# Kernel optimization log

Measured on AMD Instinct MI355X. Metric: run time of the kernel, lower is better.

## Reference

```python
import jax, jax.numpy as jnp
import numpy as np
from jax import lax

B, S, T = 256, 128, 64
IN, MID, HID = 4, 128, 512
NH = 4  # attention heads


def setup_inputs() -> dict:
    key = jax.random.key(0)
    ks = iter(jax.random.split(key, 64))
    def p(*shape):
        return jax.random.normal(next(ks), shape, jnp.float32) * 0.05
    d = {}
    d["src"] = jax.random.normal(next(ks), (B, S, IN), jnp.float32)
    d["trg"] = jax.random.normal(next(ks), (B, T, IN), jnp.float32)
    # fc_in: IN -> MID//4 -> MID//2 -> MID
    d["fi_w1"] = p(MID // 4, IN); d["fi_b1"] = p(MID // 4)
    d["fi_w2"] = p(MID // 2, MID // 4); d["fi_b2"] = p(MID // 2)
    d["fi_w3"] = p(MID, MID // 2); d["fi_b3"] = p(MID)
    # encoder: 2-layer bidirectional LSTM (layer0 in=MID, layer1 in=2*HID)
    for name, ind in [("e0", MID), ("e1", 2 * HID)]:
        for sfx in ["f", "b"]:
            d[name + sfx + "_wih"] = p(4 * HID, ind)
            d[name + sfx + "_whh"] = p(4 * HID, HID)
            d[name + sfx + "_bih"] = p(4 * HID)
            d[name + sfx + "_bhh"] = p(4 * HID)
    d["attnfc_w"] = p(MID, 2 * HID); d["attnfc_b"] = p(MID)
    d["inproj_w"] = p(3 * MID, MID); d["inproj_b"] = p(3 * MID)
    d["outproj_w"] = p(MID, MID); d["outproj_b"] = p(MID)
    # decoder: 2-layer unidirectional LSTM (layer0 in=MID, layer1 in=HID)
    for name, ind in [("d0", MID), ("d1", HID)]:
        d[name + "_wih"] = p(4 * HID, ind)
        d[name + "_whh"] = p(4 * HID, HID)
        d[name + "_bih"] = p(4 * HID)
        d[name + "_bhh"] = p(4 * HID)
    # fc_out: HID -> MID//2 -> MID//4 -> IN
    d["fo_w1"] = p(MID // 2, HID); d["fo_b1"] = p(MID // 2)
    d["fo_w2"] = p(MID // 4, MID // 2); d["fo_b2"] = p(MID // 4)
    d["fo_w3"] = p(IN, MID // 4); d["fo_b3"] = p(IN)
    return d


def _gelu(x):
    return jax.nn.gelu(x, approximate=False)  # torch default GELU is exact


def _mlp3(x, w1, b1, w2, b2, w3, b3):
    h = _gelu(x @ w1.T + b1)
    h = _gelu(h @ w2.T + b2)
    return h @ w3.T + b3


def _lstm(x, h0, c0, wih, whh, bih, bhh, reverse=False):
    """PyTorch-semantics LSTM layer. x: (B,T,in) -> (hs (B,T,H), h_T, c_T)."""
    xg = jnp.einsum('bti,gi->btg', x, wih) + (bih + bhh)  # fold input GEMM over time
    def step(carry, xt):
        h, c = carry
        g = xt + h @ whh.T
        i, f, gg, o = jnp.split(g, 4, axis=-1)  # torch gate order: i,f,g,o
        c = jax.nn.sigmoid(f) * c + jax.nn.sigmoid(i) * jnp.tanh(gg)
        h = jax.nn.sigmoid(o) * jnp.tanh(c)
        return (h, c), h
    (h, c), hs = lax.scan(step, (h0, c0), jnp.swapaxes(xg, 0, 1), reverse=reverse)
    return jnp.swapaxes(hs, 0, 1), h, c


def _mha(q_in, kv, inproj_w, inproj_b, outproj_w, outproj_b):
    E = q_in.shape[-1]
    dh = E // NH
    wq, wk, wv = jnp.split(inproj_w, 3, axis=0)
    bq, bk, bv = jnp.split(inproj_b, 3)
    q = q_in @ wq.T + bq
    k = kv @ wk.T + bk
    v = kv @ wv.T + bv
    hd = lambda x: x.reshape(x.shape[0], x.shape[1], NH, dh)
    scores = jnp.einsum('bqhd,bkhd->bhqk', hd(q), hd(k)) * (1.0 / float(np.sqrt(dh)))
    a = jax.nn.softmax(scores, axis=-1)
    o = jnp.einsum('bhqk,bkhd->bqhd', a, hd(v)).reshape(q.shape)
    return o @ outproj_w.T + outproj_b


def reference(src, trg,
              fi_w1, fi_b1, fi_w2, fi_b2, fi_w3, fi_b3,
              e0f_wih, e0f_whh, e0f_bih, e0f_bhh, e0b_wih, e0b_whh, e0b_bih, e0b_bhh,
              e1f_wih, e1f_whh, e1f_bih, e1f_bhh, e1b_wih, e1b_whh, e1b_bih, e1b_bhh,
              attnfc_w, attnfc_b, inproj_w, inproj_b, outproj_w, outproj_b,
              d0_wih, d0_whh, d0_bih, d0_bhh, d1_wih, d1_whh, d1_bih, d1_bhh,
              fo_w1, fo_b1, fo_w2, fo_b2, fo_w3, fo_b3):
    bsz = src.shape[0]
    z = jnp.zeros((bsz, HID), src.dtype)
    enc_embed = _mlp3(src, fi_w1, fi_b1, fi_w2, fi_b2, fi_w3, fi_b3)
    # encoder layer 0 (bidirectional)
    l0f, hf0, cf0 = _lstm(enc_embed, z, z, e0f_wih, e0f_whh, e0f_bih, e0f_bhh)
    l0b, hb0, cb0 = _lstm(enc_embed, z, z, e0b_wih, e0b_whh, e0b_bih, e0b_bhh, reverse=True)
    x1 = jnp.concatenate([l0f, l0b], axis=-1)
    # encoder layer 1 (bidirectional)
    l1f, hf1, cf1 = _lstm(x1, z, z, e1f_wih, e1f_whh, e1f_bih, e1f_bhh)
    l1b, hb1, cb1 = _lstm(x1, z, z, e1b_wih, e1b_whh, e1b_bih, e1b_bhh, reverse=True)
    enc_out = jnp.concatenate([l1f, l1b], axis=-1)  # (B,S,2H)
    # h.view(L,2,B,H).sum(dim=1): sum forward+backward final states per layer
    h_l0, c_l0 = hf0 + hb0, cf0 + cb0
    h_l1, c_l1 = hf1 + hb1, cf1 + cb1
    proj_enc = jnp.tanh(enc_out @ attnfc_w.T + attnfc_b)  # (B,S,MID)
    # teacher_forcing_ratio = 1.0 -> decoder inputs are exactly trg[:, 0:T]
    inp = _mlp3(trg, fi_w1, fi_b1, fi_w2, fi_b2, fi_w3, fi_b3)  # (B,T,MID)
    attn_out = _mha(inp, proj_enc, inproj_w, inproj_b, outproj_w, outproj_b)
    dec_input = inp + attn_out
    d0, _, _ = _lstm(dec_input, h_l0, c_l0, d0_wih, d0_whh, d0_bih, d0_bhh)
    d1, _, _ = _lstm(d0, h_l1, c_l1, d1_wih, d1_whh, d1_bih, d1_bhh)
    delta = _mlp3(d1, fo_w1, fo_b1, fo_w2, fo_b2, fo_w3, fo_b3)
    return trg + delta  # pred_t = trg[:, t-1] + delta_t
```

## Files before the change

### kernel.cpp

```cpp
#include <hip/hip_runtime.h>
#include <cstdint>
#include <cstddef>
#include <cstdio>

typedef __bf16 bf16;
typedef __bf16 bf16x8 __attribute__((ext_vector_type(8)));
typedef __bf16 bf16x4 __attribute__((ext_vector_type(4)));
typedef float f32x4 __attribute__((ext_vector_type(4)));

#define DEVFN __device__ __forceinline__

DEVFN float geluf(float x) { return 0.5f * x * (1.0f + erff(x * 0.70710678118654752f)); }
DEVFN float sigmoidf(float x) { return 1.0f / (1.0f + expf(-x)); }

template <int WGM, int WGN, int ACT, bool RES>
__launch_bounds__(WGM * WGN * 64)
__global__ void gemm_bt(const bf16* __restrict__ A, const bf16* __restrict__ W,
                        const float* __restrict__ bias, const bf16* __restrict__ Rsd,
                        bf16* __restrict__ C, int M, int N, int K) {
  constexpr int BM = WGM * 64, BN = WGN * 64, T = WGM * WGN * 64;
  constexpr int NA = BM * 4 / T, NB = BN * 4 / T;
  __shared__ __align__(16) char ldsA[BM * 64];
  __shared__ __align__(16) char ldsB[BN * 64];
  const int tid = threadIdx.x;
  const int lane = tid & 63, wave = tid >> 6;
  const int wm = wave % WGM, wn = wave / WGM;
  const int l16 = lane & 15, quad = lane >> 4;
  const int bm0 = blockIdx.x * BM, bn0 = blockIdx.y * BN;

  f32x4 acc[4][4] = {};
  for (int k0 = 0; k0 < K; k0 += 32) {
    bf16x8 ta[NA], tb[NB];
#pragma unroll
    for (int i = 0; i < NA; ++i) {
      int lin = i * T + tid;
      int row = lin >> 2, seg = lin & 3;
      ta[i] = *(const bf16x8*)(A + (size_t)(bm0 + row) * K + k0 + seg * 8);
    }
#pragma unroll
    for (int i = 0; i < NB; ++i) {
      int lin = i * T + tid;
      int row = lin >> 2, seg = lin & 3;
      tb[i] = *(const bf16x8*)(W + (size_t)(bn0 + row) * K + k0 + seg * 8);
    }
#pragma unroll
    for (int i = 0; i < NA; ++i) *(bf16x8*)(ldsA + (i * T + tid) * 16) = ta[i];
#pragma unroll
    for (int i = 0; i < NB; ++i) *(bf16x8*)(ldsB + (i * T + tid) * 16) = tb[i];
    __syncthreads();
    bf16x8 af[4], bfrag[4];
#pragma unroll
    for (int mi = 0; mi < 4; ++mi)
      af[mi] = *(const bf16x8*)(ldsA + (wm * 64 + mi * 16 + l16) * 64 + quad * 16);
#pragma unroll
    for (int ni = 0; ni < 4; ++ni)
      bfrag[ni] = *(const bf16x8*)(ldsB + (wn * 64 + ni * 16 + l16) * 64 + quad * 16);
#pragma unroll
    for (int mi = 0; mi < 4; ++mi)
#pragma unroll
      for (int ni = 0; ni < 4; ++ni)
        acc[mi][ni] = __builtin_amdgcn_mfma_f32_16x16x32_bf16(af[mi], bfrag[ni], acc[mi][ni], 0, 0, 0);
    __syncthreads();
  }
#pragma unroll
  for (int mi = 0; mi < 4; ++mi) {
#pragma unroll
    for (int ni = 0; ni < 4; ++ni) {
      int col = bn0 + wn * 64 + ni * 16 + l16;
      float bv = bias[col];
#pragma unroll
      for (int r = 0; r < 4; ++r) {
        int row = bm0 + wm * 64 + mi * 16 + quad * 4 + r;
        float x = acc[mi][ni][r] + bv;
        if (ACT == 1) x = tanhf(x);
        if (ACT == 2) x = geluf(x);
        size_t idx = (size_t)row * N + col;
        if (RES) x += (float)Rsd[idx];
        C[idx] = (bf16)x;
      }
    }
  }
}

template <int WGM, int WGN, int ACT>
__launch_bounds__(WGM * WGN * 64)
__global__ void gemm_hcA(const bf16* __restrict__ HC, int tbase, const bf16* __restrict__ W,
                         const float* __restrict__ bias, bf16* __restrict__ C,
                         int M, int N, int K) {
  constexpr int BM = WGM * 64, BN = WGN * 64, T = WGM * WGN * 64;
  constexpr int NA = BM * 4 / T, NB = BN * 4 / T;
  __shared__ __align__(16) char ldsA[BM * 64];
  __shared__ __align__(16) char ldsB[BN * 64];
  const int tid = threadIdx.x;
  const int lane = tid & 63, wave = tid >> 6;
  const int wm = wave % WGM, wn = wave / WGM;
  const int l16 = lane & 15, quad = lane >> 4;
  const int bm0 = blockIdx.x * BM, bn0 = blockIdx.y * BN;

  f32x4 acc[4][4] = {};
  for (int k0 = 0; k0 < K; k0 += 32) {
    bf16x8 ta[NA], tb[NB];
#pragma unroll
    for (int i = 0; i < NA; ++i) {
      int lin = i * T + tid;
      int row = bm0 + (lin >> 2), seg = lin & 3;
      int t = tbase + (row >> 8), b = row & 255;
      ta[i] = *(const bf16x8*)(HC + (size_t)t * 262144 + (size_t)((k0 >> 3) + seg) * 2048 + b * 8);
    }
#pragma unroll
    for (int i = 0; i < NB; ++i) {
      int lin = i * T + tid;
      int row = lin >> 2, seg = lin & 3;
      tb[i] = *(const bf16x8*)(W + (size_t)(bn0 + row) * K + k0 + seg * 8);
    }
#pragma unroll
    for (int i = 0; i < NA; ++i) *(bf16x8*)(ldsA + (i * T + tid) * 16) = ta[i];
#pragma unroll
    for (int i = 0; i < NB; ++i) *(bf16x8*)(ldsB + (i * T + tid) * 16) = tb[i];
    __syncthreads();
    bf16x8 af[4], bfrag[4];
#pragma unroll
    for (int mi = 0; mi < 4; ++mi)
      af[mi] = *(const bf16x8*)(ldsA + (wm * 64 + mi * 16 + l16) * 64 + quad * 16);
#pragma unroll
    for (int ni = 0; ni < 4; ++ni)
      bfrag[ni] = *(const bf16x8*)(ldsB + (wn * 64 + ni * 16 + l16) * 64 + quad * 16);
#pragma unroll
    for (int mi = 0; mi < 4; ++mi)
#pragma unroll
      for (int ni = 0; ni < 4; ++ni)
        acc[mi][ni] = __builtin_amdgcn_mfma_f32_16x16x32_bf16(af[mi], bfrag[ni], acc[mi][ni], 0, 0, 0);
    __syncthreads();
  }
#pragma unroll
  for (int mi = 0; mi < 4; ++mi) {
#pragma unroll
    for (int ni = 0; ni < 4; ++ni) {
      int col = bn0 + wn * 64 + ni * 16 + l16;
      float bv = bias[col];
#pragma unroll
      for (int r = 0; r < 4; ++r) {
        int row = bm0 + wm * 64 + mi * 16 + quad * 4 + r;
        float x = acc[mi][ni][r] + bv;
        if (ACT == 1) x = tanhf(x);
        if (ACT == 2) x = geluf(x);
        C[(size_t)row * N + col] = (bf16)x;
      }
    }
  }
}

__launch_bounds__(128)
__global__ void gemm_hc_fcout(const bf16* __restrict__ HC, const bf16* __restrict__ W,
                              const float* __restrict__ bias, bf16* __restrict__ C,
                              int M, int N, int K) {
  constexpr int WGM = 2, WGN = 1;
  constexpr int BM = WGM * 64, BN = WGN * 64, T = WGM * WGN * 64;
  constexpr int NA = BM * 4 / T, NB = BN * 4 / T;
  __shared__ __align__(16) char ldsA[BM * 64];
  __shared__ __align__(16) char ldsB[BN * 64];
  const int tid = threadIdx.x;
  const int lane = tid & 63, wave = tid >> 6;
  const int wm = wave % WGM, wn = wave / WGM;
  const int l16 = lane & 15, quad = lane >> 4;
  const int bm0 = blockIdx.x * BM, bn0 = blockIdx.y * BN;

  f32x4 acc[4][4] = {};
  for (int k0 = 0; k0 < K; k0 += 32) {
    bf16x8 ta[NA], tb[NB];
#pragma unroll
    for (int i = 0; i < NA; ++i) {
      int lin = i * T + tid;
      int row = bm0 + (lin >> 2), seg = lin & 3;
      int t = row >> 8, b = row & 255;
      ta[i] = *(const bf16x8*)(HC + (size_t)t * 131072 + (size_t)((k0 >> 3) + seg) * 2048 + b * 8);
    }
#pragma unroll
    for (int i = 0; i < NB; ++i) {
      int lin = i * T + tid;
      int row = lin >> 2, seg = lin & 3;
      tb[i] = *(const bf16x8*)(W + (size_t)(bn0 + row) * K + k0 + seg * 8);
    }
#pragma unroll
    for (int i = 0; i < NA; ++i) *(bf16x8*)(ldsA + (i * T + tid) * 16) = ta[i];
#pragma unroll
    for (int i = 0; i < NB; ++i) *(bf16x8*)(ldsB + (i * T + tid) * 16) = tb[i];
    __syncthreads();
    bf16x8 af[4], bfrag[4];
#pragma unroll
    for (int mi = 0; mi < 4; ++mi)
      af[mi] = *(const bf16x8*)(ldsA + (wm * 64 + mi * 16 + l16) * 64 + quad * 16);
#pragma unroll
    for (int ni = 0; ni < 4; ++ni)
      bfrag[ni] = *(const bf16x8*)(ldsB + (wn * 64 + ni * 16 + l16) * 64 + quad * 16);
#pragma unroll
    for (int mi = 0; mi < 4; ++mi)
#pragma unroll
      for (int ni = 0; ni < 4; ++ni)
        acc[mi][ni] = __builtin_amdgcn_mfma_f32_16x16x32_bf16(af[mi], bfrag[ni], acc[mi][ni], 0, 0, 0);
    __syncthreads();
  }
#pragma unroll
  for (int mi = 0; mi < 4; ++mi) {
#pragma unroll
    for (int ni = 0; ni < 4; ++ni) {
      int col = bn0 + wn * 64 + ni * 16 + l16;
      float bv = bias[col];
#pragma unroll
      for (int r = 0; r < 4; ++r) {
        int row = bm0 + wm * 64 + mi * 16 + quad * 4 + r;
        float x = geluf(acc[mi][ni][r] + bv);
        C[(size_t)row * N + col] = (bf16)x;
      }
    }
  }
}

template <int HCMODE>
DEVFN void xg_tile(const bf16* __restrict__ A, int tbase, const bf16* __restrict__ W,
                   const float* __restrict__ bias, bf16* __restrict__ C,
                   int K, int bm0, int bn0, int tid, bf16* ldsA, bf16* ldsB) {
  const int lane = tid & 63, wave = tid >> 6;
  const int wm = wave & 1, wn = wave >> 1;
  const int l16 = lane & 15, quad = lane >> 4;
  f32x4 acc[4][4] = {};
  for (int k0 = 0; k0 < K; k0 += 32) {
    bf16x8 ta, tb0, tb1;
    {
      int row = bm0 + (tid >> 2), seg = tid & 3;
      if (HCMODE) {
        int t = tbase + (row >> 8), b = row & 255;
        ta = *(const bf16x8*)(A + (size_t)t * 262144 + (size_t)((k0 >> 3) + seg) * 2048 + b * 8);
      } else {
        ta = *(const bf16x8*)(A + (size_t)row * K + k0 + seg * 8);
      }
    }
    { int row = tid >> 2, seg = tid & 3;
      tb0 = *(const bf16x8*)(W + (size_t)(bn0 + row) * K + k0 + seg * 8); }
    { int lin = 512 + tid; int row = lin >> 2, seg = lin & 3;
      tb1 = *(const bf16x8*)(W + (size_t)(bn0 + row) * K + k0 + seg * 8); }
    *(bf16x8*)(ldsA + tid * 8) = ta;
    *(bf16x8*)(ldsB + tid * 8) = tb0;
    *(bf16x8*)(ldsB + (512 + tid) * 8) = tb1;
    __syncthreads();
    bf16x8 af[4], bfr[4];
#pragma unroll
    for (int mi = 0; mi < 4; ++mi)
      af[mi] = *(const bf16x8*)(ldsA + (wm * 64 + mi * 16 + l16) * 32 + quad * 8);
#pragma unroll
    for (int ni = 0; ni < 4; ++ni)
      bfr[ni] = *(const bf16x8*)(ldsB + (wn * 64 + ni * 16 + l16) * 32 + quad * 8);
#pragma unroll
    for (int mi = 0; mi < 4; ++mi)
#pragma unroll
      for (int ni = 0; ni < 4; ++ni)
        acc[mi][ni] = __builtin_amdgcn_mfma_f32_16x16x32_bf16(af[mi], bfr[ni], acc[mi][ni], 0, 0, 0);
    __syncthreads();
  }
#pragma unroll
  for (int mi = 0; mi < 4; ++mi) {
#pragma unroll
    for (int ni = 0; ni < 4; ++ni) {
      int col = bn0 + wn * 64 + ni * 16 + l16;
      float bv = bias[col];
#pragma unroll
      for (int r = 0; r < 4; ++r) {
        int row = bm0 + wm * 64 + mi * 16 + quad * 4 + r;
        C[(size_t)row * 2048 + col] = (bf16)(acc[mi][ni][r] + bv);
      }
    }
  }
}

struct RDir {
  const bf16* whh_r;
  const bf16* xg;
  bf16* hc;
  int slcOff, rev;
  const bf16* h0;
  float* cbuf;
  bf16* hfin;
};

struct GJob {
  int mode;
  const bf16* Af; const bf16* Ab;
  int tbF, tbB;
  const bf16* Wf; const bf16* Wb;
  const float* bsF; const float* bsB;
  bf16* outF; bf16* outB;
};

__launch_bounds__(512, 1)
__global__ void lstm_rec_g(RDir da, RDir db, int t0, int tc, int Tfull,
                           int* __restrict__ cnts, GJob job) {
  __shared__ __align__(16) char smem[36864];
  const int blk = blockIdx.x;
  const int tid = threadIdx.x;

  if (blk >= 128) {
    if (job.mode == 0) return;
    bf16* ldsA = (bf16*)smem;
    bf16* ldsB = (bf16*)(smem + 8192);
    const int gb = blk - 128;
    const int K = (job.mode == 2) ? 1024 : 128;
    for (int tile = gb; tile < 512; tile += 128) {
      int dir = tile >> 8;
      int rem = tile & 255;
      int mi = rem >> 3, ni = rem & 7;
      const bf16* A = dir ? job.Ab : job.Af;
      int tb = dir ? job.tbB : job.tbF;
      const bf16* W = dir ? job.Wb : job.Wf;
      const float* bs = dir ? job.bsB : job.bsF;
      bf16* C = dir ? job.outB : job.outF;
      if (job.mode == 2)
        xg_tile<1>(A, tb, W, bs, C, K, mi * 128, ni * 256, tid, ldsA, ldsB);
      else
        xg_tile<0>(A, tb, W, bs, C, K, mi * 128, ni * 256, tid, ldsA, ldsB);
    }
    return;
  }

  bf16* whh_lds = (bf16*)smem;
  bf16* hstg = (bf16*)(smem + 32768);
  const RDir d = (blk >= 64) ? db : da;
  const int slice = blk & 63;
  const int colBase = slice * 32, unitBase = slice * 8;
  const int w = tid >> 6, lane = tid & 63;
  const int l16 = lane & 15, quad = lane >> 4;

  for (int e = tid * 8; e < 32 * 512; e += 512 * 8) {
    int c = e >> 9, k0 = e & 511;
    bf16x8 v = *(const bf16x8*)(d.whh_r + (size_t)(colBase + c) * 512 + k0);
    *(bf16x8*)(whh_lds + ((k0 >> 3) << 8) + (c << 3)) = v;
  }
  float cst[2][2];
#pragma unroll
  for (int m = 0; m < 2; ++m)
#pragma unroll
    for (int i = 0; i < 2; ++i) {
      int b = (w * 2 + i) * 16 + l16;
      cst[m][i] = d.cbuf[(size_t)b * 512 + unitBase + m * 4 + quad];
    }
  __syncthreads();

  int* cnt = cnts + (blk & 64);
  const int b0 = (w * 2) * 16 + l16;
  const int b1 = b0 + 16;

  for (int s = 0; s < tc; ++s) {
    const int sg = t0 + s;
    const int t = d.rev ? (Tfull - 1 - sg) : sg;
    const int lt = d.rev ? (tc - 1 - s) : s;

    bf16x4 gxr[2][2];
#pragma unroll
    for (int m = 0; m < 2; ++m)
#pragma unroll
      for (int i = 0; i < 2; ++i) {
        int b = b0 + i * 16;
        gxr[m][i] = *(const bf16x4*)(d.xg + ((size_t)lt * 256 + b) * 2048 + colBase + m * 16 + quad * 4);
      }
    bf16x8 hr[16][2];
    if (sg == 0) {
      const bf16* hp0 = d.h0 + (size_t)b0 * 512 + quad * 8;
      const bf16* hp1 = d.h0 + (size_t)b1 * 512 + quad * 8;
#pragma unroll
      for (int kk = 0; kk < 16; ++kk) {
        hr[kk][0] = *(const bf16x8*)(hp0 + kk * 32);
        hr[kk][1] = *(const bf16x8*)(hp1 + kk * 32);
      }
    } else {
      const int tp = d.rev ? (t + 1) : (t - 1);
      const bf16* hc = d.hc + (size_t)tp * 262144 + (size_t)d.slcOff * 2048;
#pragma unroll
      for (int kk = 0; kk < 16; ++kk) {
        int u8 = kk * 4 + quad;
        hr[kk][0] = *(const bf16x8*)(hc + u8 * 2048 + (size_t)b0 * 8);
        hr[kk][1] = *(const bf16x8*)(hc + u8 * 2048 + (size_t)b1 * 8);
      }
    }
    __builtin_amdgcn_sched_barrier(0);

    f32x4 acc[2][2] = {};
#pragma unroll
    for (int kk = 0; kk < 16; ++kk) {
      bf16x8 a0 = *(const bf16x8*)(whh_lds + kk * 1024 + quad * 256 + l16 * 8);
      bf16x8 a1 = *(const bf16x8*)(whh_lds + kk * 1024 + quad * 256 + 128 + l16 * 8);
      acc[0][0] = __builtin_amdgcn_mfma_f32_16x16x32_bf16(a0, hr[kk][0], acc[0][0], 0, 0, 0);
      acc[1][0] = __builtin_amdgcn_mfma_f32_16x16x32_bf16(a1, hr[kk][0], acc[1][0], 0, 0, 0);
      acc[0][1] = __builtin_amdgcn_mfma_f32_16x16x32_bf16(a0, hr[kk][1], acc[0][1], 0, 0, 0);
      acc[1][1] = __builtin_amdgcn_mfma_f32_16x16x32_bf16(a1, hr[kk][1], acc[1][1], 0, 0, 0);
    }
#pragma unroll
    for (int m = 0; m < 2; ++m)
#pragma unroll
      for (int i = 0; i < 2; ++i) {
        float gi = acc[m][i][0] + (float)gxr[m][i][0];
        float gf = acc[m][i][1] + (float)gxr[m][i][1];
        float gg = acc[m][i][2] + (float)gxr[m][i][2];
        float go = acc[m][i][3] + (float)gxr[m][i][3];
        float cn = sigmoidf(gf) * cst[m][i] + sigmoidf(gi) * tanhf(gg);
        float hv = sigmoidf(go) * tanhf(cn);
        cst[m][i] = cn;
        int b = (w * 2 + i) * 16 + l16;
        hstg[b * 8 + m * 4 + quad] = (bf16)hv;
      }
    __syncthreads();
    {
      unsigned long long v = *(const unsigned long long*)(hstg + tid * 4);
      __hip_atomic_store((unsigned long long*)(d.hc + (size_t)t * 262144 +
                                               (size_t)(d.slcOff + slice) * 2048 + tid * 4),
                         v, __ATOMIC_RELAXED, __HIP_MEMORY_SCOPE_AGENT);
    }
    __syncthreads();
    if (s < tc - 1 && tid == 0)
      __hip_atomic_fetch_add(cnt, 1, __ATOMIC_RELAXED, __HIP_MEMORY_SCOPE_AGENT);
    if (sg == Tfull - 1 && d.hfin && tid < 256) {
      const unsigned long long* p = (const unsigned long long*)(hstg + tid * 8);
      unsigned long long* r2 = (unsigned long long*)(d.hfin + (size_t)tid * 512 + unitBase);
      r2[0] = p[0]; r2[1] = p[1];
    }
    if (s < tc - 1) {
      if (w == 0) {
        int target = 64 * (s + 1), guard = 0;
        while (__hip_atomic_load(cnt, __ATOMIC_RELAXED, __HIP_MEMORY_SCOPE_AGENT) < target) {
          __builtin_amdgcn_s_sleep(2);
          if (++guard > (1 << 22)) break;
        }
      }
      __syncthreads();
    }
  }
#pragma unroll
  for (int m = 0; m < 2; ++m)
#pragma unroll
    for (int i = 0; i < 2; ++i) {
      int b = (w * 2 + i) * 16 + l16;
      d.cbuf[(size_t)b * 512 + unitBase + m * 4 + quad] = cst[m][i];
    }
}

__launch_bounds__(512, 1)
__global__ void lstm_dec_fused(
    const bf16* __restrict__ whh0, const bf16* __restrict__ xg0,
    bf16* __restrict__ hc0, const bf16* __restrict__ h0d0, float* __restrict__ c0buf,
    const bf16* __restrict__ whh1, const bf16* __restrict__ wih1, const float* __restrict__ bias1,
    bf16* __restrict__ hc1, const bf16* __restrict__ h0d1,
    float* __restrict__ c1buf, int* __restrict__ cnts) {
  const int blk = blockIdx.x;
  const int tid = threadIdx.x;
  const int w = tid >> 6, lane = tid & 63;
  const int l16 = lane & 15, quad = lane >> 4;
  constexpr int TC = 64;

  __shared__ __align__(16) bf16 wldsA[32 * 512];
  __shared__ __align__(16) bf16 wldsB[32 * 512];
  __shared__ __align__(16) bf16 hstg[128 * 8];

  int* cnt0 = cnts;
  int* cnt1 = cnts + 64;

  if (blk < 128) {
    const int slice = blk >> 1, bh = blk & 1;
    const int colBase = slice * 32;
    const int b0 = bh * 128 + w * 16 + l16;
    for (int e = tid * 8; e < 32 * 512; e += 512 * 8) {
      int c = e >> 9, k0 = e & 511;
      bf16x8 v = *(const bf16x8*)(whh0 + (size_t)(colBase + c) * 512 + k0);
      *(bf16x8*)(wldsA + ((k0 >> 3) << 8) + (c << 3)) = v;
    }
    float cst[2];
#pragma unroll
    for (int m = 0; m < 2; ++m)
      cst[m] = c0buf[(size_t)b0 * 512 + slice * 8 + m * 4 + quad];
    __syncthreads();

    for (int s = 0; s < TC; ++s) {
      bf16x4 gxr[2];
#pragma unroll
      for (int m = 0; m < 2; ++m)
        gxr[m] = *(const bf16x4*)(xg0 + ((size_t)s * 256 + b0) * 2048 + colBase + m * 16 + quad * 4);
      bf16x8 hr[16];
      if (s == 0) {
        const bf16* hp = h0d0 + (size_t)b0 * 512 + quad * 8;
#pragma unroll
        for (int kk = 0; kk < 16; ++kk) hr[kk] = *(const bf16x8*)(hp + kk * 32);
      } else {
        const bf16* hc = hc0 + (size_t)(s - 1) * 131072;
#pragma unroll
        for (int kk = 0; kk < 16; ++kk) {
          int u8 = kk * 4 + quad;
          hr[kk] = *(const bf16x8*)(hc + u8 * 2048 + (size_t)b0 * 8);
        }
      }
      __builtin_amdgcn_sched_barrier(0);
      f32x4 acc[2] = {};
#pragma unroll
      for (int kk = 0; kk < 16; ++kk) {
        bf16x8 a0 = *(const bf16x8*)(wldsA + kk * 1024 + quad * 256 + l16 * 8);
        bf16x8 a1 = *(const bf16x8*)(wldsA + kk * 1024 + quad * 256 + 128 + l16 * 8);
        acc[0] = __builtin_amdgcn_mfma_f32_16x16x32_bf16(a0, hr[kk], acc[0], 0, 0, 0);
        acc[1] = __builtin_amdgcn_mfma_f32_16x16x32_bf16(a1, hr[kk], acc[1], 0, 0, 0);
      }
#pragma unroll
      for (int m = 0; m < 2; ++m) {
        float gi = acc[m][0] + (float)gxr[m][0];
        float gf = acc[m][1] + (float)gxr[m][1];
        float gg = acc[m][2] + (float)gxr[m][2];
        float go = acc[m][3] + (float)gxr[m][3];
        float cn = sigmoidf(gf) * cst[m] + sigmoidf(gi) * tanhf(gg);
        float hv = sigmoidf(go) * tanhf(cn);
        cst[m] = cn;
        int lb = w * 16 + l16;
        hstg[lb * 8 + m * 4 + quad] = (bf16)hv;
      }
      __syncthreads();
      if (tid < 256) {
        unsigned long long v = *(const unsigned long long*)(hstg + tid * 4);
        __hip_atomic_store((unsigned long long*)(hc0 + (size_t)s * 131072 +
                                                 slice * 2048 + bh * 1024 + tid * 4),
                           v, __ATOMIC_RELAXED, __HIP_MEMORY_SCOPE_AGENT);
      }
      __syncthreads();
      if (tid == 0)
        __hip_atomic_fetch_add(cnt0, 1, __ATOMIC_RELAXED, __HIP_MEMORY_SCOPE_AGENT);
      if (s < TC - 1) {
        if (w == 0) {
          int target = 128 * (s + 1), guard = 0;
          while (__hip_atomic_load(cnt0, __ATOMIC_RELAXED, __HIP_MEMORY_SCOPE_AGENT) < target) {
            __builtin_amdgcn_s_sleep(2);
            if (++guard > (1 << 22)) break;
          }
        }
        __syncthreads();
      }
    }
#pragma unroll
    for (int m = 0; m < 2; ++m)
      c0buf[(size_t)b0 * 512 + slice * 8 + m * 4 + quad] = cst[m];
  } else {
    const int idx = blk - 128, slice = idx >> 1, bh = idx & 1;
    const int colBase = slice * 32;
    const int b0 = bh * 128 + w * 16 + l16;
    for (int e = tid * 8; e < 32 * 512; e += 512 * 8) {
      int c = e >> 9, k0 = e & 511;
      bf16x8 v = *(const bf16x8*)(whh1 + (size_t)(colBase + c) * 512 + k0);
      *(bf16x8*)(wldsA + ((k0 >> 3) << 8) + (c << 3)) = v;
      bf16x8 u = *(const bf16x8*)(wih1 + (size_t)(colBase + c) * 512 + k0);
      *(bf16x8*)(wldsB + ((k0 >> 3) << 8) + (c << 3)) = u;
    }
    float gbv[2][4];
#pragma unroll
    for (int m = 0; m < 2; ++m)
#pragma unroll
      for (int r = 0; r < 4; ++r) gbv[m][r] = bias1[colBase + m * 16 + quad * 4 + r];
    float cst[2];
#pragma unroll
    for (int m = 0; m < 2; ++m)
      cst[m] = c1buf[(size_t)b0 * 512 + slice * 8 + m * 4 + quad];
    __syncthreads();
    if (w == 0) {
      int guard = 0;
      while (__hip_atomic_load(cnt0, __ATOMIC_RELAXED, __HIP_MEMORY_SCOPE_AGENT) < 128) {
        __builtin_amdgcn_s_sleep(2);
        if (++guard > (1 << 22)) break;
      }
    }
    __syncthreads();

    for (int s = 0; s < TC; ++s) {
      bf16x8 hr[16], xr[16];
      if (s == 0) {
        const bf16* hp = h0d1 + (size_t)b0 * 512 + quad * 8;
#pragma unroll
        for (int kk = 0; kk < 16; ++kk) hr[kk] = *(const bf16x8*)(hp + kk * 32);
      } else {
        const bf16* hc = hc1 + (size_t)(s - 1) * 131072;
#pragma unroll
        for (int kk = 0; kk < 16; ++kk) {
          int u8 = kk * 4 + quad;
          hr[kk] = *(const bf16x8*)(hc + u8 * 2048 + (size_t)b0 * 8);
        }
      }
      {
        const bf16* xc = hc0 + (size_t)s * 131072;
#pragma unroll
        for (int kk = 0; kk < 16; ++kk) {
          int u8 = kk * 4 + quad;
          xr[kk] = *(const bf16x8*)(xc + u8 * 2048 + (size_t)b0 * 8);
        }
      }
      __builtin_amdgcn_sched_barrier(0);
      f32x4 acc[2] = {};
#pragma unroll
      for (int kk = 0; kk < 16; ++kk) {
        bf16x8 a0 = *(const bf16x8*)(wldsA + kk * 1024 + quad * 256 + l16 * 8);
        bf16x8 a1 = *(const bf16x8*)(wldsA + kk * 1024 + quad * 256 + 128 + l16 * 8);
        acc[0] = __builtin_amdgcn_mfma_f32_16x16x32_bf16(a0, hr[kk], acc[0], 0, 0, 0);
        acc[1] = __builtin_amdgcn_mfma_f32_16x16x32_bf16(a1, hr[kk], acc[1], 0, 0, 0);
      }
#pragma unroll
      for (int kk = 0; kk < 16; ++kk) {
        bf16x8 aw0 = *(const bf16x8*)(wldsB + kk * 1024 + quad * 256 + l16 * 8);
        bf16x8 aw1 = *(const bf16x8*)(wldsB + kk * 1024 + quad * 256 + 128 + l16 * 8);
        acc[0] = __builtin_amdgcn_mfma_f32_16x16x32_bf16(aw0, xr[kk], acc[0], 0, 0, 0);
        acc[1] = __builtin_amdgcn_mfma_f32_16x16x32_bf16(aw1, xr[kk], acc[1], 0, 0, 0);
      }
#pragma unroll
      for (int m = 0; m < 2; ++m) {
        float gi = acc[m][0] + gbv[m][0];
        float gf = acc[m][1] + gbv[m][1];
        float gg = acc[m][2] + gbv[m][2];
        float go = acc[m][3] + gbv[m][3];
        float cn = sigmoidf(gf) * cst[m] + sigmoidf(gi) * tanhf(gg);
        float hv = sigmoidf(go) * tanhf(cn);
        cst[m] = cn;
        int lb = w * 16 + l16;
        hstg[lb * 8 + m * 4 + quad] = (bf16)hv;
      }
      __syncthreads();
      if (tid < 256) {
        unsigned long long v = *(const unsigned long long*)(hstg + tid * 4);
        __hip_atomic_store((unsigned long long*)(hc1 + (size_t)s * 131072 +
                                                 slice * 2048 + bh * 1024 + tid * 4),
                           v, __ATOMIC_RELAXED, __HIP_MEMORY_SCOPE_AGENT);
      }
      __syncthreads();
      if (s < TC - 1) {
        if (tid == 0)
          __hip_atomic_fetch_add(cnt1, 1, __ATOMIC_RELAXED, __HIP_MEMORY_SCOPE_AGENT);
        if (w == 0) {
          int t1 = 128 * (s + 1), t0n = 128 * (s + 2), guard = 0;
          while (true) {
            int v1 = __hip_atomic_load(cnt1, __ATOMIC_RELAXED, __HIP_MEMORY_SCOPE_AGENT);
            int v0 = __hip_atomic_load(cnt0, __ATOMIC_RELAXED, __HIP_MEMORY_SCOPE_AGENT);
            if (v1 >= t1 && v0 >= t0n) break;
            __builtin_amdgcn_s_sleep(2);
            if (++guard > (1 << 22)) break;
          }
        }
        __syncthreads();
      }
    }
#pragma unroll
    for (int m = 0; m < 2; ++m)
      c1buf[(size_t)b0 * 512 + slice * 8 + m * 4 + quad] = cst[m];
  }
}

__launch_bounds__(256)
__global__ void fc_in_mlp(const float* __restrict__ x, bf16* __restrict__ y, int rows, int tmod,
                          const float* __restrict__ w1, const float* __restrict__ b1,
                          const float* __restrict__ w2, const float* __restrict__ b2,
                          const float* __restrict__ w3, const float* __restrict__ b3) {
  __shared__ float sm[10592];
  const int tid = threadIdx.x;
  for (int i = tid; i < 10592; i += 256) {
    float v;
    if (i < 128) v = w1[i];
    else if (i < 160) v = b1[i - 128];
    else if (i < 2208) v = w2[i - 160];
    else if (i < 2272) v = b2[i - 2208];
    else if (i < 10464) v = w3[i - 2272];
    else v = b3[i - 10464];
    sm[i] = v;
  }
  __syncthreads();
  int row = blockIdx.x * 256 + tid;
  if (row >= rows) return;
  int orow = tmod ? ((row % tmod) * 256 + row / tmod) : row;
  float xin[4];
#pragma unroll
  for (int k = 0; k < 4; ++k) xin[k] = x[(size_t)row * 4 + k];
  float h1[32];
#pragma unroll
  for (int j = 0; j < 32; ++j) {
    float a = sm[128 + j];
#pragma unroll
    for (int k = 0; k < 4; ++k) a += sm[j * 4 + k] * xin[k];
    h1[j] = geluf(a);
  }
  float h2[64];
#pragma unroll
  for (int j = 0; j < 64; ++j) {
    float a = sm[2208 + j];
#pragma unroll
    for (int k = 0; k < 32; ++k) a += sm[160 + j * 32 + k] * h1[k];
    h2[j] = geluf(a);
  }
  for (int c = 0; c < 8; ++c) {
    float accv[16];
#pragma unroll
    for (int j = 0; j < 16; ++j) accv[j] = sm[10464 + c * 16 + j];
#pragma unroll
    for (int j = 0; j < 16; ++j) {
#pragma unroll
      for (int k = 0; k < 64; ++k) accv[j] += sm[2272 + (c * 16 + j) * 64 + k] * h2[k];
    }
#pragma unroll
    for (int j = 0; j < 16; ++j) y[(size_t)orow * 128 + c * 16 + j] = (bf16)accv[j];
  }
}

__launch_bounds__(256)
__global__ void fc_out_tail(const bf16* __restrict__ h1in, const float* __restrict__ trg,
                            float* __restrict__ out, int rows,
                            const float* __restrict__ w2, const float* __restrict__ b2,
                            const float* __restrict__ w3, const float* __restrict__ b3) {
  __shared__ float sm[2212];
  const int tid = threadIdx.x;
  for (int i = tid; i < 2212; i += 256) {
    float v;
    if (i < 2048) v = w2[i];
    else if (i < 2080) v = b2[i - 2048];
    else if (i < 2208) v = w3[i - 2080];
    else v = b3[i - 2208];
    sm[i] = v;
  }
  __syncthreads();
  int row = blockIdx.x * 256 + tid;
  if (row >= rows) return;
  int b = row >> 6, t = row & 63;
  const bf16* h1p = h1in + ((size_t)t * 256 + b) * 64;
  float h1[64];
#pragma unroll
  for (int k = 0; k < 64; ++k) h1[k] = (float)h1p[k];
  float h2[32];
#pragma unroll
  for (int j = 0; j < 32; ++j) {
    float a = sm[2048 + j];
#pragma unroll
    for (int k = 0; k < 64; ++k) a += sm[j * 64 + k] * h1[k];
    h2[j] = geluf(a);
  }
#pragma unroll
  for (int dd = 0; dd < 4; ++dd) {
    float a = sm[2208 + dd];
#pragma unroll
    for (int k = 0; k < 32; ++k) a += sm[2080 + dd * 32 + k] * h2[k];
    out[(size_t)row * 4 + dd] = trg[(size_t)row * 4 + dd] + a;
  }
}

__launch_bounds__(128)
__global__ void attention_kernel(const bf16* __restrict__ Q, const bf16* __restrict__ K,
                                 const bf16* __restrict__ V, bf16* __restrict__ O) {
  __shared__ bf16 qs[64 * 32];
  __shared__ float ks[128 * 33];
  __shared__ bf16 vs[128 * 32];
  __shared__ float sc[64 * 132];
  const int b = blockIdx.x, h = blockIdx.y, tid = threadIdx.x;
  for (int i = tid; i < 64 * 32; i += 128) {
    int t = i >> 5, dd = i & 31;
    qs[i] = Q[((size_t)t * 256 + b) * 128 + h * 32 + dd];
  }
  for (int i = tid; i < 128 * 32; i += 128) {
    int s = i >> 5, dd = i & 31;
    size_t ridx = ((size_t)s * 256 + b) * 128 + h * 32 + dd;
    ks[s * 33 + dd] = (float)K[ridx];
    vs[i] = V[ridx];
  }
  __syncthreads();
  const float scale = 0.17677669529663687f;
  for (int i = tid; i < 64 * 128; i += 128) {
    int t = i >> 7, s = i & 127;
    float a = 0.f;
#pragma unroll
    for (int dd = 0; dd < 32; ++dd) a += (float)qs[t * 32 + dd] * ks[s * 33 + dd];
    sc[t * 132 + s] = a * scale;
  }
  __syncthreads();
  if (tid < 64) {
    float m = -1e30f;
    for (int s = 0; s < 128; ++s) m = fmaxf(m, sc[tid * 132 + s]);
    float sum = 0.f;
    for (int s = 0; s < 128; ++s) { float e = expf(sc[tid * 132 + s] - m); sc[tid * 132 + s] = e; sum += e; }
    float r = 1.0f / sum;
    for (int s = 0; s < 128; ++s) sc[tid * 132 + s] *= r;
  }
  __syncthreads();
  for (int i = tid; i < 64 * 32; i += 128) {
    int t = i >> 5, dd = i & 31;
    float a = 0.f;
    for (int s = 0; s < 128; ++s) a += sc[t * 132 + s] * (float)vs[s * 32 + dd];
    O[((size_t)t * 256 + b) * 128 + h * 32 + dd] = (bf16)a;
  }
}

__global__ void reorder_gate_rows(const float* __restrict__ in, bf16* __restrict__ out, int K) {
  int i = blockIdx.x * 256 + threadIdx.x;
  if (i >= 2048 * K) return;
  int r = i / K, k = i - r * K;
  int nr = 4 * (r & 511) + (r >> 9);
  out[(size_t)nr * K + k] = (bf16)in[i];
}

__global__ void combine_bias(const float* __restrict__ a, const float* __restrict__ b,
                             float* __restrict__ out) {
  int i = blockIdx.x * 256 + threadIdx.x;
  if (i >= 2048) return;
  out[4 * (i & 511) + (i >> 9)] = a[i] + b[i];
}

__global__ void f2b(const float* __restrict__ in, bf16* __restrict__ out, int n) {
  int i = blockIdx.x * 256 + threadIdx.x;
  if (i < n) out[i] = (bf16)in[i];
}

__global__ void zero_u32(uint32_t* __restrict__ p, int n) {
  int i = blockIdx.x * 256 + threadIdx.x;
  if (i < n) p[i] = 0u;
}

__global__ void dec_state_init(const bf16* __restrict__ hf, const bf16* __restrict__ hb,
                               const float* __restrict__ cf, const float* __restrict__ cb,
                               bf16* __restrict__ hout, float* __restrict__ cout) {
  int i = blockIdx.x * 256 + threadIdx.x;
  if (i >= 256 * 512) return;
  hout[i] = (bf16)((float)hf[i] + (float)hb[i]);
  cout[i] = cf[i] + cb[i];
}

extern "C" void kernel_launch(void* const* d_in, const int* in_sizes, int n_in,
                              void* d_out, int out_size, void* d_ws, size_t ws_size,
                              hipStream_t stream) {
  (void)in_sizes; (void)n_in; (void)out_size;
  const float* src = (const float*)d_in[0];
  const float* trg = (const float*)d_in[1];
  const float* fi_w1 = (const float*)d_in[2];
  const float* fi_b1 = (const float*)d_in[3];
  const float* fi_w2 = (const float*)d_in[4];
  const float* fi_b2 = (const float*)d_in[5];
  const float* fi_w3 = (const float*)d_in[6];
  const float* fi_b3 = (const float*)d_in[7];
  const float* wih_in[6] = {(const float*)d_in[8],  (const float*)d_in[12], (const float*)d_in[16],
                            (const float*)d_in[20], (const float*)d_in[30], (const float*)d_in[34]};
  const float* whh_in[6] = {(const float*)d_in[9],  (const float*)d_in[13], (const float*)d_in[17],
                            (const float*)d_in[21], (const float*)d_in[31], (const float*)d_in[35]};
  const float* bih_in[6] = {(const float*)d_in[10], (const float*)d_in[14], (const float*)d_in[18],
                            (const float*)d_in[22], (const float*)d_in[32], (const float*)d_in[36]};
  const float* bhh_in[6] = {(const float*)d_in[11], (const float*)d_in[15], (const float*)d_in[19],
                            (const float*)d_in[23], (const float*)d_in[33], (const float*)d_in[37]};
  const int kin[6] = {128, 128, 1024, 1024, 128, 512};
  const float* attnfc_w = (const float*)d_in[24];
  const float* attnfc_b = (const float*)d_in[25];
  const float* inproj_w = (const float*)d_in[26];
  const float* inproj_b = (const float*)d_in[27];
  const float* outproj_w = (const float*)d_in[28];
  const float* outproj_b = (const float*)d_in[29];
  const float* fo_w1 = (const float*)d_in[38];
  const float* fo_b1 = (const float*)d_in[39];
  const float* fo_w2 = (const float*)d_in[40];
  const float* fo_b2 = (const float*)d_in[41];
  const float* fo_w3 = (const float*)d_in[42];
  const float* fo_b3 = (const float*)d_in[43];
  float* out = (float*)d_out;

  char* base = (char*)d_ws;
  size_t o = 0;
  auto take = [&](size_t bytes) -> char* {
    char* p = base + o;
    o = (o + bytes + 255) & ~(size_t)255;
    return p;
  };
  bf16* wr_wih[6]; for (int i = 0; i < 6; ++i) wr_wih[i] = (bf16*)take((size_t)2048 * kin[i] * 2);
  bf16* wr_whh[6]; for (int i = 0; i < 6; ++i) wr_whh[i] = (bf16*)take((size_t)2048 * 512 * 2);
  float* bias_l[6]; for (int i = 0; i < 6; ++i) bias_l[i] = (float*)take(2048 * 4);
  bf16* attnfc_wb = (bf16*)take((size_t)128 * 1024 * 2);
  bf16* inproj_wb = (bf16*)take((size_t)384 * 128 * 2);
  bf16* outproj_wb = (bf16*)take((size_t)128 * 128 * 2);
  bf16* fo_w1b = (bf16*)take((size_t)64 * 512 * 2);
  bf16* h0_0 = (bf16*)take((size_t)6 * 256 * 512 * 2);
  bf16* hf_0 = (bf16*)take((size_t)6 * 256 * 512 * 2);
  float* c_0 = (float*)take((size_t)6 * 256 * 512 * 4);
  int* flags = (int*)take(4096 * 4);
  bf16* h0_[6]; bf16* hf_[6]; float* c_[6];
  for (int i = 0; i < 6; ++i) {
    h0_[i] = h0_0 + (size_t)i * 256 * 512;
    hf_[i] = hf_0 + (size_t)i * 256 * 512;
    c_[i] = c_0 + (size_t)i * 256 * 512;
  }
  char* RA = take((size_t)64 << 20);
  char* RB = take((size_t)64 << 20);
  char* XG = take((size_t)64 << 20);
  bf16* embed = (bf16*)take((size_t)32768 * 128 * 2);
  size_t required = o;
  if (required > ws_size) {
    fprintf(stderr, "[kernel_launch] ws_size=%zu < required=%zu — aborting launch\n",
            ws_size, required);
    return;
  }

  bf16* x1_hc    = (bf16*)RA;
  bf16* proj_enc = (bf16*)RA;
  bf16* inp      = (bf16*)(RA + ((size_t)8 << 20));
  bf16* qb       = (bf16*)(RA + ((size_t)12 << 20));
  bf16* kb       = (bf16*)(RA + ((size_t)16 << 20));
  bf16* vb       = (bf16*)(RA + ((size_t)24 << 20));
  bf16* attnb    = (bf16*)(RA + ((size_t)32 << 20));
  bf16* dec_in   = (bf16*)(RA + ((size_t)36 << 20));
  bf16* fc1out   = (bf16*)(RA + ((size_t)40 << 20));
  bf16* enc_hc   = (bf16*)RB;
  bf16* hc0      = (bf16*)RB;
  bf16* hc1      = (bf16*)(RB + ((size_t)20 << 20));
  bf16* bufF[2]  = {(bf16*)XG, (bf16*)(XG + ((size_t)32 << 20))};
  bf16* bufB[2]  = {(bf16*)(XG + ((size_t)16 << 20)), (bf16*)(XG + ((size_t)48 << 20))};
  bf16* xg_dec   = (bf16*)XG;

  for (int i = 0; i < 6; ++i) {
    reorder_gate_rows<<<dim3((2048 * kin[i] + 255) / 256), 256, 0, stream>>>(wih_in[i], wr_wih[i], kin[i]);
    reorder_gate_rows<<<dim3(4096), 256, 0, stream>>>(whh_in[i], wr_whh[i], 512);
    combine_bias<<<dim3(8), 256, 0, stream>>>(bih_in[i], bhh_in[i], bias_l[i]);
  }
  f2b<<<dim3(512), 256, 0, stream>>>(attnfc_w, attnfc_wb, 128 * 1024);
  f2b<<<dim3(192), 256, 0, stream>>>(inproj_w, inproj_wb, 384 * 128);
  f2b<<<dim3(64), 256, 0, stream>>>(outproj_w, outproj_wb, 128 * 128);
  f2b<<<dim3(128), 256, 0, stream>>>(fo_w1, fo_w1b, 64 * 512);
  zero_u32<<<dim3(1024), 256, 0, stream>>>((uint32_t*)h0_0, 4 * 256 * 512 / 2);
  zero_u32<<<dim3(2048), 256, 0, stream>>>((uint32_t*)c_0, 4 * 256 * 512);
  zero_u32<<<dim3(16), 256, 0, stream>>>((uint32_t*)flags, 4096);

  fc_in_mlp<<<dim3(128), 256, 0, stream>>>(src, embed, 32768, 128, fi_w1, fi_b1, fi_w2, fi_b2, fi_w3, fi_b3);

  constexpr int TCC = 16, NCH = 8;
  gemm_bt<2, 2, 0, false><<<dim3(32, 16), 256, 0, stream>>>(
      embed, wr_wih[0], bias_l[0], nullptr, bufF[0], 4096, 2048, 128);
  gemm_bt<2, 2, 0, false><<<dim3(32, 16), 256, 0, stream>>>(
      embed + (size_t)(128 - TCC) * 256 * 128, wr_wih[1], bias_l[1], nullptr, bufB[0], 4096, 2048, 128);
  for (int c = 0; c < NCH; ++c) {
    GJob job{};
    if (c < NCH - 1) {
      int n = c + 1;
      job.mode = 1;
      job.Af = embed + (size_t)(TCC * n) * 256 * 128;
      job.Ab = embed + (size_t)(128 - TCC * n - TCC) * 256 * 128;
      job.Wf = wr_wih[0]; job.Wb = wr_wih[1];
      job.bsF = bias_l[0]; job.bsB = bias_l[1];
      job.outF = bufF[n & 1]; job.outB = bufB[n & 1];
    }
    RDir f{wr_whh[0], bufF[c & 1], x1_hc, 0, 0, h0_[0], c_[0], hf_[0]};
    RDir bk{wr_whh[1], bufB[c & 1], x1_hc, 64, 1, h0_[1], c_[1], hf_[1]};
    lstm_rec_g<<<dim3(256), 512, 0, stream>>>(f, bk, c * TCC, TCC, 128, flags + c * 128, job);
  }
  gemm_hcA<2, 2, 0><<<dim3(32, 16), 256, 0, stream>>>(
      x1_hc, 0, wr_wih[2], bias_l[2], bufF[0], 4096, 2048, 1024);
  gemm_hcA<2, 2, 0><<<dim3(32, 16), 256, 0, stream>>>(
      x1_hc, 128 - TCC, wr_wih[3], bias_l[3], bufB[0], 4096, 2048, 1024);
  for (int c = 0; c < NCH; ++c) {
    GJob job{};
    if (c < NCH - 1) {
      int n = c + 1;
      job.mode = 2;
      job.Af = x1_hc; job.Ab = x1_hc;
      job.tbF = TCC * n; job.tbB = 128 - TCC * n - TCC;
      job.Wf = wr_wih[2]; job.Wb = wr_wih[3];
      job.bsF = bias_l[2]; job.bsB = bias_l[3];
      job.outF = bufF[n & 1]; job.outB = bufB[n & 1];
    }
    RDir f{wr_whh[2], bufF[c & 1], enc_hc, 0, 0, h0_[2], c_[2], hf_[2]};
    RDir bk{wr_whh[3], bufB[c & 1], enc_hc, 64, 1, h0_[3], c_[3], hf_[3]};
    lstm_rec_g<<<dim3(256), 512, 0, stream>>>(f, bk, c * TCC, TCC, 128, flags + 1024 + c * 128, job);
  }

  gemm_hcA<2, 2, 1><<<dim3(256, 1), 256, 0, stream>>>(
      enc_hc, 0, attnfc_wb, attnfc_b, proj_enc, 32768, 128, 1024);

  fc_in_mlp<<<dim3(64), 256, 0, stream>>>(trg, inp, 16384, 64, fi_w1, fi_b1, fi_w2, fi_b2, fi_w3, fi_b3);

  gemm_bt<2, 2, 0, false><<<dim3(128, 1), 256, 0, stream>>>(inp, inproj_wb, inproj_b, nullptr, qb, 16384, 128, 128);
  gemm_bt<2, 2, 0, false><<<dim3(256, 1), 256, 0, stream>>>(proj_enc, inproj_wb + (size_t)128 * 128, inproj_b + 128, nullptr, kb, 32768, 128, 128);
  gemm_bt<2, 2, 0, false><<<dim3(256, 1), 256, 0, stream>>>(proj_enc, inproj_wb + (size_t)256 * 128, inproj_b + 256, nullptr, vb, 32768, 128, 128);
  attention_kernel<<<dim3(256, 4), 128, 0, stream>>>(qb, kb, vb, attnb);
  gemm_bt<2, 2, 0, true><<<dim3(128, 1), 256, 0, stream>>>(attnb, outproj_wb, outproj_b, inp, dec_in, 16384, 128, 128);

  dec_state_init<<<dim3(512), 256, 0, stream>>>(hf_[0], hf_[1], c_[0], c_[1], h0_[4], c_[4]);
  dec_state_init<<<dim3(512), 256, 0, stream>>>(hf_[2], hf_[3], c_[2], c_[3], h0_[5], c_[5]);

  gemm_bt<2, 2, 0, false><<<dim3(128, 16), 256, 0, stream>>>(dec_in, wr_wih[4], bias_l[4], nullptr, xg_dec, 16384, 2048, 128);
  lstm_dec_fused<<<dim3(256), 512, 0, stream>>>(
      wr_whh[4], xg_dec, hc0, h0_[4], c_[4],
      wr_whh[5], wr_wih[5], bias_l[5], hc1, h0_[5], c_[5],
      flags + 2048);

  gemm_hc_fcout<<<dim3(128, 1), 128, 0, stream>>>(hc1, fo_w1b, fo_b1, fc1out, 16384, 64, 512);
  fc_out_tail<<<dim3(64), 256, 0, stream>>>(fc1out, trg, out, 16384, fo_w2, fo_b2, fo_w3, fo_b3);
}
```

Before: 3.055 ms.

## Repartition encoder LSTM recurrence blocks by batch half and wider unit slice

Each of the 64 recurrent blocks per direction now owns 16 hidden units (64 gate columns) for half of the batch, where before it owned 8 units for the whole batch. The W_hh slice held in LDS doubles to 64 KB, and each wave keeps one batch tile of h registers with four accumulator tiles instead of two by two. The aim is to halve the h-vector bytes each block reads from global memory per timestep, at the cost of twice the LDS per block and a more complex scatter when writing h.

New measurement: 2.917 ms. 4.5% less time.

```diff
diff --git a/kernel.cpp b/kernel.cpp
--- a/kernel.cpp
+++ b/kernel.cpp
@@ -294,7 +294,7 @@
 __launch_bounds__(512, 1)
 __global__ void lstm_rec_g(RDir da, RDir db, int t0, int tc, int Tfull,
                            int* __restrict__ cnts, GJob job) {
-  __shared__ __align__(16) char smem[36864];
+  __shared__ __align__(16) char smem[69632];
   const int blk = blockIdx.x;
   const int tid = threadIdx.x;
 
@@ -322,104 +322,94 @@
   }
 
   bf16* whh_lds = (bf16*)smem;
-  bf16* hstg = (bf16*)(smem + 32768);
-  const RDir d = (blk >= 64) ? db : da;
-  const int slice = blk & 63;
-  const int colBase = slice * 32, unitBase = slice * 8;
+  bf16* hstg = (bf16*)(smem + 65536);
+  const int isB = (blk >= 64);
+  const RDir d = isB ? db : da;
+  const int idx = blk & 63;
+  const int bslice = idx >> 1, bh = idx & 1;
+  const int colBase = bslice * 64, unitBase = bslice * 16;
   const int w = tid >> 6, lane = tid & 63;
   const int l16 = lane & 15, quad = lane >> 4;
-
-  for (int e = tid * 8; e < 32 * 512; e += 512 * 8) {
+  const int b0 = bh * 128 + w * 16 + l16;
+
+  for (int e = tid * 8; e < 64 * 512; e += 512 * 8) {
     int c = e >> 9, k0 = e & 511;
     bf16x8 v = *(const bf16x8*)(d.whh_r + (size_t)(colBase + c) * 512 + k0);
-    *(bf16x8*)(whh_lds + ((k0 >> 3) << 8) + (c << 3)) = v;
-  }
-  float cst[2][2];
-#pragma unroll
-  for (int m = 0; m < 2; ++m)
-#pragma unroll
-    for (int i = 0; i < 2; ++i) {
-      int b = (w * 2 + i) * 16 + l16;
-      cst[m][i] = d.cbuf[(size_t)b * 512 + unitBase + m * 4 + quad];
-    }
+    *(bf16x8*)(whh_lds + ((k0 >> 3) << 9) + (c << 3)) = v;
+  }
+  float cst[4];
+#pragma unroll
+  for (int m = 0; m < 4; ++m)
+    cst[m] = d.cbuf[(size_t)b0 * 512 + unitBase + m * 4 + quad];
   __syncthreads();
 
-  int* cnt = cnts + (blk & 64);
-  const int b0 = (w * 2) * 16 + l16;
-  const int b1 = b0 + 16;
+  int* cnt = cnts + (isB ? 64 : 0);
 
   for (int s = 0; s < tc; ++s) {
     const int sg = t0 + s;
     const int t = d.rev ? (Tfull - 1 - sg) : sg;
     const int lt = d.rev ? (tc - 1 - s) : s;
 
-    bf16x4 gxr[2][2];
-#pragma unroll
-    for (int m = 0; m < 2; ++m)
-#pragma unroll
-      for (int i = 0; i < 2; ++i) {
-        int b = b0 + i * 16;
-        gxr[m][i] = *(const bf16x4*)(d.xg + ((size_t)lt * 256 + b) * 2048 + colBase + m * 16 + quad * 4);
-      }
-    bf16x8 hr[16][2];
+    bf16x4 gxr[4];
+#pragma unroll
+    for (int m = 0; m < 4; ++m)
+      gxr[m] = *(const bf16x4*)(d.xg + ((size_t)lt * 256 + b0) * 2048 + colBase + m * 16 + quad * 4);
+    bf16x8 hr[16];
     if (sg == 0) {
-      const bf16* hp0 = d.h0 + (size_t)b0 * 512 + quad * 8;
-      const bf16* hp1 = d.h0 + (size_t)b1 * 512 + quad * 8;
-#pragma unroll
-      for (int kk = 0; kk < 16; ++kk) {
-        hr[kk][0] = *(const bf16x8*)(hp0 + kk * 32);
-        hr[kk][1] = *(const bf16x8*)(hp1 + kk * 32);
-      }
+      const bf16* hp = d.h0 + (size_t)b0 * 512 + quad * 8;
+#pragma unroll
+      for (int kk = 0; kk < 16; ++kk) hr[kk] = *(const bf16x8*)(hp + kk * 32);
     } else {
       const int tp = d.rev ? (t + 1) : (t - 1);
       const bf16* hc = d.hc + (size_t)tp * 262144 + (size_t)d.slcOff * 2048;
 #pragma unroll
       for (int kk = 0; kk < 16; ++kk) {
         int u8 = kk * 4 + quad;
-        hr[kk][0] = *(const bf16x8*)(hc + u8 * 2048 + (size_t)b0 * 8);
-        hr[kk][1] = *(const bf16x8*)(hc + u8 * 2048 + (size_t)b1 * 8);
+        hr[kk] = *(const bf16x8*)(hc + u8 * 2048 + (size_t)b0 * 8);
       }
     }
     __builtin_amdgcn_sched_barrier(0);
 
-    f32x4 acc[2][2] = {};
+    f32x4 acc[4] = {};
 #pragma unroll
     for (int kk = 0; kk < 16; ++kk) {
-      bf16x8 a0 = *(const bf16x8*)(whh_lds + kk * 1024 + quad * 256 + l16 * 8);
-      bf16x8 a1 = *(const bf16x8*)(whh_lds + kk * 1024 + quad * 256 + 128 + l16 * 8);
-      acc[0][0] = __builtin_amdgcn_mfma_f32_16x16x32_bf16(a0, hr[kk][0], acc[0][0], 0, 0, 0);
-      acc[1][0] = __builtin_amdgcn_mfma_f32_16x16x32_bf16(a1, hr[kk][0], acc[1][0], 0, 0, 0);
-      acc[0][1] = __builtin_amdgcn_mfma_f32_16x16x32_bf16(a0, hr[kk][1], acc[0][1], 0, 0, 0);
-      acc[1][1] = __builtin_amdgcn_mfma_f32_16x16x32_bf16(a1, hr[kk][1], acc[1][1], 0, 0, 0);
-    }
-#pragma unroll
-    for (int m = 0; m < 2; ++m)
-#pragma unroll
-      for (int i = 0; i < 2; ++i) {
-        float gi = acc[m][i][0] + (float)gxr[m][i][0];
-        float gf = acc[m][i][1] + (float)gxr[m][i][1];
-        float gg = acc[m][i][2] + (float)gxr[m][i][2];
-        float go = acc[m][i][3] + (float)gxr[m][i][3];
-        float cn = sigmoidf(gf) * cst[m][i] + sigmoidf(gi) * tanhf(gg);
-        float hv = sigmoidf(go) * tanhf(cn);
-        cst[m][i] = cn;
-        int b = (w * 2 + i) * 16 + l16;
-        hstg[b * 8 + m * 4 + quad] = (bf16)hv;
-      }
+      bf16x8 a0 = *(const bf16x8*)(whh_lds + kk * 2048 + quad * 512 + l16 * 8);
+      bf16x8 a1 = *(const bf16x8*)(whh_lds + kk * 2048 + quad * 512 + 128 + l16 * 8);
+      bf16x8 a2 = *(const bf16x8*)(whh_lds + kk * 2048 + quad * 512 + 256 + l16 * 8);
+      bf16x8 a3 = *(const bf16x8*)(whh_lds + kk * 2048 + quad * 512 + 384 + l16 * 8);
+      acc[0] = __builtin_amdgcn_mfma_f32_16x16x32_bf16(a0, hr[kk], acc[0], 0, 0, 0);
+      acc[1] = __builtin_amdgcn_mfma_f32_16x16x32_bf16(a1, hr[kk], acc[1], 0, 0, 0);
+      acc[2] = __builtin_amdgcn_mfma_f32_16x16x32_bf16(a2, hr[kk], acc[2], 0, 0, 0);
+      acc[3] = __builtin_amdgcn_mfma_f32_16x16x32_bf16(a3, hr[kk], acc[3], 0, 0, 0);
+    }
+#pragma unroll
+    for (int m = 0; m < 4; ++m) {
+      float gi = acc[m][0] + (float)gxr[m][0];
+      float gf = acc[m][1] + (float)gxr[m][1];
+      float gg = acc[m][2] + (float)gxr[m][2];
+      float go = acc[m][3] + (float)gxr[m][3];
+      float cn = sigmoidf(gf) * cst[m] + sigmoidf(gi) * tanhf(gg);
+      float hv = sigmoidf(go) * tanhf(cn);
+      cst[m] = cn;
+      int lb = w * 16 + l16;
+      hstg[lb * 16 + m * 4 + quad] = (bf16)hv;
+    }
     __syncthreads();
     {
-      unsigned long long v = *(const unsigned long long*)(hstg + tid * 4);
+      int hi = tid >> 8, r = tid & 255, lb = r >> 1, uh = r & 1;
+      unsigned long long v = *(const unsigned long long*)(hstg + lb * 16 + hi * 8 + uh * 4);
       __hip_atomic_store((unsigned long long*)(d.hc + (size_t)t * 262144 +
-                                               (size_t)(d.slcOff + slice) * 2048 + tid * 4),
+                                               (size_t)(d.slcOff + 2 * bslice + hi) * 2048 +
+                                               bh * 1024 + lb * 8 + uh * 4),
                          v, __ATOMIC_RELAXED, __HIP_MEMORY_SCOPE_AGENT);
     }
     __syncthreads();
     if (s < tc - 1 && tid == 0)
       __hip_atomic_fetch_add(cnt, 1, __ATOMIC_RELAXED, __HIP_MEMORY_SCOPE_AGENT);
-    if (sg == Tfull - 1 && d.hfin && tid < 256) {
-      const unsigned long long* p = (const unsigned long long*)(hstg + tid * 8);
-      unsigned long long* r2 = (unsigned long long*)(d.hfin + (size_t)tid * 512 + unitBase);
-      r2[0] = p[0]; r2[1] = p[1];
+    if (sg == Tfull - 1 && d.hfin) {
+      int hi = tid >> 8, r = tid & 255, lb = r >> 1, uh = r & 1;
+      const unsigned long long* p = (const unsigned long long*)(hstg + lb * 16 + hi * 8 + uh * 4);
+      *(unsigned long long*)(d.hfin + (size_t)(bh * 128 + lb) * 512 + unitBase + hi * 8 + uh * 4) = p[0];
     }
     if (s < tc - 1) {
       if (w == 0) {
@@ -433,12 +423,8 @@
     }
   }
 #pragma unroll
-  for (int m = 0; m < 2; ++m)
-#pragma unroll
-    for (int i = 0; i < 2; ++i) {
-      int b = (w * 2 + i) * 16 + l16;
-      d.cbuf[(size_t)b * 512 + unitBase + m * 4 + quad] = cst[m][i];
-    }
+  for (int m = 0; m < 4; ++m)
+    d.cbuf[(size_t)b0 * 512 + unitBase + m * 4 + quad] = cst[m];
 }
 
 __launch_bounds__(512, 1)
```
